# Performance work log

Measured on AMD Instinct MI355X. Metric: run time of the kernel, lower is better.

Reference implementation:

```python
import jax, jax.numpy as jnp
import numpy as np

T, B, H, I = 128, 32, 256, 256


def setup_inputs() -> dict:
    key = jax.random.key(0)
    ks = jax.random.split(key, 8)
    s = 0.05
    embs = jax.random.normal(ks[0], (T, B, I), jnp.float32)
    lens = jax.random.randint(ks[1], (B,), 1, T + 1)  # lengths in [1, T]
    W_ih = jax.random.normal(ks[2], (4 * H, I), jnp.float32) * s
    W_hh = jax.random.normal(ks[3], (4 * H, H), jnp.float32) * s
    b_ih = jax.random.normal(ks[4], (4 * H,), jnp.float32) * s
    b_hh = jax.random.normal(ks[5], (4 * H,), jnp.float32) * s
    W_a = jax.random.normal(ks[6], (H, 2 * H), jnp.float32) * s  # attention combine (Luong-style)
    b_a = jax.random.normal(ks[7], (H,), jnp.float32) * s
    return {"embs": embs, "lens": lens, "W_ih": W_ih, "W_hh": W_hh,
            "b_ih": b_ih, "b_hh": b_hh, "W_a": W_a, "b_a": b_a}


def reference(embs, lens, W_ih, W_hh, b_ih, b_hh, W_a, b_a):
    Tn, Bn, _ = embs.shape
    Hn = W_hh.shape[1]
    t_idx = jnp.arange(Tn)

    def step(carry, inp):
        h, c, buf, h_fin, c_fin = carry  # h,c: [B,H]; buf: [T,B,H] history of outputs
        t, emb = inp
        # dot-product attention of current hidden over past outputs (steps < t)
        scores = jnp.einsum('tbh,bh->tb', buf, h)
        valid = (t_idx < t)[:, None]
        alpha = jax.nn.softmax(jnp.where(valid, scores, -1e9), axis=0)
        ctx = jnp.einsum('tb,tbh->bh', alpha, buf)
        h_att = jnp.tanh(jnp.concatenate([ctx, h], axis=-1) @ W_a.T + b_a)
        h = jnp.where(t > 0, h_att, h)  # no history at t=0
        # standard PyTorch LSTM cell (gate order i,f,g,o)
        gates = emb @ W_ih.T + b_ih + h @ W_hh.T + b_hh
        i_g, f_g, g_g, o_g = jnp.split(gates, 4, axis=-1)
        c = jax.nn.sigmoid(f_g) * c + jax.nn.sigmoid(i_g) * jnp.tanh(g_g)
        h = jax.nn.sigmoid(o_g) * jnp.tanh(c)
        buf = buf.at[t].set(h)
        take = (t == lens - 1)[:, None]
        h_fin = jnp.where(take, h, h_fin)
        c_fin = jnp.where(take, c, c_fin)
        return (h, c, buf, h_fin, c_fin), h

    z = jnp.zeros((Bn, Hn), embs.dtype)
    buf0 = jnp.zeros((Tn, Bn, Hn), embs.dtype)
    carry, output = jax.lax.scan(step, (z, z, buf0, z, z), (t_idx, embs))
    # output: [T,B,H]; final (h,c) gathered at t == lens-1: [B,H]
    return output, carry[3], carry[4]
```

## Files before the change

kernel.cpp:

```cpp
#include <hip/hip_runtime.h>


#define T_DIM 128
#define B_DIM 32

typedef _Float16 half2_t __attribute__((ext_vector_type(2)));

static __device__ __forceinline__ unsigned pack2(float a, float b) {
  half2_t h;
  h.x = (_Float16)a;
  h.y = (_Float16)b;
  return __builtin_bit_cast(unsigned, h);
}

static __device__ __forceinline__ float dot2f(unsigned w, unsigned v, float acc) {
  half2_t a = __builtin_bit_cast(half2_t, w);
  half2_t b = __builtin_bit_cast(half2_t, v);
#if __has_builtin(__builtin_amdgcn_fdot2)
  return __builtin_amdgcn_fdot2(a, b, acc, false);
#else
  return acc + (float)a.x * (float)b.x + (float)a.y * (float)b.y;
#endif
}

static __device__ __forceinline__ float dot8(uint4 w, uint4 v, float acc) {
  acc = dot2f(w.x, v.x, acc);
  acc = dot2f(w.y, v.y, acc);
  acc = dot2f(w.z, v.z, acc);
  acc = dot2f(w.w, v.w, acc);
  return acc;
}

static __device__ __forceinline__ float lo16(unsigned u) {
  return (float)__builtin_bit_cast(half2_t, u).x;
}
static __device__ __forceinline__ float hi16(unsigned u) {
  return (float)__builtin_bit_cast(half2_t, u).y;
}

static __device__ __forceinline__ float fsig(float x) {
  return __builtin_amdgcn_rcpf(1.f + __expf(-x));
}
static __device__ __forceinline__ float ftanh(float x) {
  float e = __expf(2.f * x);
  return 1.f - 2.f * __builtin_amdgcn_rcpf(e + 1.f);
}

__global__ void pack_weights(const float* __restrict__ W_ih, const float* __restrict__ W_hh,
                             const float* __restrict__ W_a, float* __restrict__ W_ihT,
                             uint4* __restrict__ Whh_pack, uint4* __restrict__ Wa_pack,
                             unsigned long long* __restrict__ ywp,
                             unsigned long long* __restrict__ psx) {
  int n = blockIdx.x * 256 + threadIdx.x;
  {
    int k = n >> 10, r = n & 1023;
    W_ihT[n] = W_ih[r * 256 + k];
  }
  if (n < 32768) {
    int m = n >> 12, tid = (n >> 3) & 511, i = n & 7;
    int r_local = tid >> 2, qk = tid & 3;
    int q = r_local >> 5, jl = r_local & 31;
    int r = q * 256 + m * 32 + jl;
    const float* src = W_hh + r * 256 + (4 * i + qk) * 8;
    uint4 v;
    v.x = pack2(src[0], src[1]);
    v.y = pack2(src[2], src[3]);
    v.z = pack2(src[4], src[5]);
    v.w = pack2(src[6], src[7]);
    Whh_pack[n] = v;
  }
  if (n < 16384) {
    int m = n >> 11, j = (n >> 3) & 255, c = n & 7;
    int col0 = (c < 4) ? (m * 32 + c * 8) : (256 + m * 32 + (c - 4) * 8);
    const float* src = W_a + j * 512 + col0;
    uint4 v;
    v.x = pack2(src[0], src[1]);
    v.y = pack2(src[2], src[3]);
    v.z = pack2(src[4], src[5]);
    v.w = pack2(src[6], src[7]);
    Wa_pack[n] = v;
  }
  if (n < 65536)
    __hip_atomic_store(&ywp[n], 0ull, __ATOMIC_RELAXED, __HIP_MEMORY_SCOPE_AGENT);
  else if (n < 81920)
    __hip_atomic_store(&psx[n - 65536], 0ull, __ATOMIC_RELAXED, __HIP_MEMORY_SCOPE_AGENT);
}

__global__ void compute_gih(const float* __restrict__ embs, const float* __restrict__ W_ihT,
                            const float* __restrict__ b_ih, const float* __restrict__ b_hh,
                            float* __restrict__ gih) {
  __shared__ float embS[8][256];
  const int tid = threadIdx.x;
  const int tb0 = blockIdx.x * 8;
#pragma unroll
  for (int e = 0; e < 8; ++e) embS[e][tid] = embs[(size_t)(tb0 + e) * 256 + tid];
  __syncthreads();
  float acc[8][4];
#pragma unroll
  for (int e = 0; e < 8; ++e)
#pragma unroll
    for (int q = 0; q < 4; ++q) acc[e][q] = 0.f;
  for (int k = 0; k < 256; ++k) {
    float w0 = W_ihT[k * 1024 + tid];
    float w1 = W_ihT[k * 1024 + tid + 256];
    float w2 = W_ihT[k * 1024 + tid + 512];
    float w3 = W_ihT[k * 1024 + tid + 768];
#pragma unroll
    for (int e = 0; e < 8; ++e) {
      float x = embS[e][k];
      acc[e][0] += x * w0;
      acc[e][1] += x * w1;
      acc[e][2] += x * w2;
      acc[e][3] += x * w3;
    }
  }
#pragma unroll
  for (int q = 0; q < 4; ++q) {
    float bias = b_ih[q * 256 + tid] + b_hh[q * 256 + tid];
#pragma unroll
    for (int e = 0; e < 8; ++e)
      gih[(size_t)(tb0 + e) * 1024 + q * 256 + tid] = acc[e][q] + bias;
  }
}

__global__ void __launch_bounds__(512, 1)
alstm_rec(const int* __restrict__ lens, const float* __restrict__ gih,
          const uint4* __restrict__ Whh_pack, const uint4* __restrict__ Wa_pack,
          const float* __restrict__ b_a, unsigned long long* __restrict__ ywp,
          unsigned long long* __restrict__ psx, float* __restrict__ out,
          float* __restrict__ hfin, float* __restrict__ cfin) {
  const int tid = threadIdx.x;
  const int b = blockIdx.x & 31;
  const int m = blockIdx.x >> 5;

  __shared__ __align__(16) unsigned histSl[128 * 18];
  __shared__ __align__(16) float ystoreF[128 * 256];
  __shared__ __align__(16) unsigned hp2[128];
  __shared__ __align__(16) unsigned hsl2[16];
  __shared__ float sc[128];
  __shared__ float zp[4][256];
  __shared__ float gsl[128];

  uint4 wh4[8];
  {
    const uint4* p = Whh_pack + ((size_t)m * 512 + tid) * 8;
#pragma unroll
    for (int i = 0; i < 8; ++i) wh4[i] = p[i];
  }
  uint4 way[4], waw[4];
  {
    const int j_pub = (tid - 128) & 255;
    const uint4* p = Wa_pack + ((size_t)m * 256 + j_pub) * 8;
#pragma unroll
    for (int i = 0; i < 4; ++i) way[i] = p[i];
#pragma unroll
    for (int i = 0; i < 4; ++i) waw[i] = p[4 + i];
  }
  const float ba_j = (tid < 256) ? b_a[tid] : 0.f;
  const int len_b = lens[b];
  const int r_local = tid >> 2, qk = tid & 3;
  const int gq = r_local >> 5, gjl = r_local & 31;

  if (tid < 128) hp2[tid] = 0u;
  float c_reg = 0.f;
  __syncthreads();

  for (int t = 0; t < T_DIM; ++t) {
    float gih_v = gih[((size_t)t * 32 + b) * 1024 + gq * 256 + m * 32 + gjl];
    float w_j = 0.f;

    if (t > 0) {
      if (tid < 256) {
        const unsigned long long* base = ywp + b * 2048 + tid;
        unsigned long long v[8];
        for (;;) {
          bool ok = true;
#pragma unroll
          for (int mm = 0; mm < 8; ++mm)
            v[mm] = __hip_atomic_load(base + mm * 256, __ATOMIC_RELAXED, __HIP_MEMORY_SCOPE_AGENT);
#pragma unroll
          for (int mm = 0; mm < 8; ++mm) ok &= ((unsigned)v[mm] == (unsigned)t);
          if (ok) break;
          __builtin_amdgcn_s_sleep(1);
        }
        float y = 0.f, w = 0.f;
#pragma unroll
        for (int mm = 0; mm < 8; ++mm) {
          unsigned pl = (unsigned)(v[mm] >> 32);
          y += lo16(pl);
          w += hi16(pl);
        }
        w_j = w;
        ystoreF[(t - 1) * 256 + tid] = y;
      } else if (tid < 320) {
        const int p = tid - 256;
        const unsigned long long* base = psx + b * 512 + p;
        unsigned long long v[8];
        for (;;) {
          bool ok = true;
#pragma unroll
          for (int mm = 0; mm < 8; ++mm)
            v[mm] = __hip_atomic_load(base + mm * 64, __ATOMIC_RELAXED, __HIP_MEMORY_SCOPE_AGENT);
#pragma unroll
          for (int mm = 0; mm < 8; ++mm) ok &= ((unsigned)v[mm] == (unsigned)t);
          if (ok) break;
          __builtin_amdgcn_s_sleep(1);
        }
        float s0 = 0.f, s1 = 0.f;
#pragma unroll
        for (int mm = 0; mm < 8; ++mm) {
          unsigned pl = (unsigned)(v[mm] >> 32);
          s0 += lo16(pl);
          s1 += hi16(pl);
        }
        sc[2 * p] = s0;
        sc[2 * p + 1] = s1;
      }
      __syncthreads();
      if (tid < 64) {
        float v0 = (tid < t) ? sc[tid] : -3.0e38f;
        float v1 = (tid + 64 < t) ? sc[tid + 64] : -3.0e38f;
        float mx = fmaxf(v0, v1);
#pragma unroll
        for (int off = 32; off >= 1; off >>= 1) mx = fmaxf(mx, __shfl_xor(mx, off));
        float e0 = (tid < t) ? __expf(v0 - mx) : 0.f;
        float e1 = (tid + 64 < t) ? __expf(v1 - mx) : 0.f;
        float sm = e0 + e1;
#pragma unroll
        for (int off = 32; off >= 1; off >>= 1) sm += __shfl_xor(sm, off);
        float inv = __builtin_amdgcn_rcpf(sm);
        sc[tid] = e0 * inv;
        sc[tid + 64] = e1 * inv;
      }
      __syncthreads();
      {
        const int sp = tid >> 7, p2 = tid & 127;
        float c0 = 0.f, c1 = 0.f;
        const float* yb = ystoreF + 2 * p2;
        for (int s = sp; s < t; s += 4) {
          float al = sc[s];
          float2 yv = *(const float2*)(yb + s * 256);
          c0 += al * yv.x;
          c1 += al * yv.y;
        }
        zp[sp][2 * p2] = c0;
        zp[sp][2 * p2 + 1] = c1;
      }
      __syncthreads();
      if (tid < 256) {
        float z = zp[0][tid] + zp[1][tid] + zp[2][tid] + zp[3][tid];
        float hv = ftanh(ba_j + w_j + z);
        float o = __shfl_xor(hv, 1);
        if (!(tid & 1)) hp2[tid >> 1] = pack2(hv, o);
      }
      __syncthreads();
    }
    {
      float a = 0.f;
#pragma unroll
      for (int i = 0; i < 8; ++i) {
        const int c = 4 * i + qk;
        uint4 hv = *(const uint4*)&hp2[c << 2];
        a = dot8(wh4[i], hv, a);
      }
      a += __shfl_xor(a, 1);
      a += __shfl_xor(a, 2);
      if (qk == 0) gsl[r_local] = a + gih_v;
    }
    __syncthreads();
    if (tid < 32) {
      float ig = fsig(gsl[tid]);
      float fg = fsig(gsl[32 + tid]);
      float gg = ftanh(gsl[64 + tid]);
      float og = fsig(gsl[96 + tid]);
      float cn = fg * c_reg + ig * gg;
      float hn = og * ftanh(cn);
      c_reg = cn;
      out[((size_t)t * 32 + b) * 256 + m * 32 + tid] = hn;
      if (t == len_b - 1) {
        hfin[b * 256 + m * 32 + tid] = hn;
        cfin[b * 256 + m * 32 + tid] = cn;
      }
      float o = __shfl_xor(hn, 1);
      if (!(tid & 1)) {
        unsigned u = pack2(hn, o);
        hsl2[tid >> 1] = u;
        histSl[t * 18 + (tid >> 1)] = u;
      }
    }
    __syncthreads();
    if (tid < 128) {
      float a = 0.f;
#pragma unroll
      for (int k = 0; k < 8; ++k) {
        uint2 hw = *(const uint2*)&histSl[tid * 18 + 2 * k];
        uint2 qv = *(const uint2*)&hsl2[2 * k];
        a = dot2f(hw.x, qv.x, a);
        a = dot2f(hw.y, qv.y, a);
      }
      float o = __shfl_xor(a, 1);
      if (!(tid & 1)) {
        unsigned long long v = ((unsigned long long)pack2(a, o) << 32) |
                               (unsigned long long)(unsigned)(t + 1);
        __hip_atomic_store(&psx[b * 512 + m * 64 + (tid >> 1)], v, __ATOMIC_RELAXED,
                           __HIP_MEMORY_SCOPE_AGENT);
      }
    } else if (tid < 384) {
      const int j = tid - 128;
      float ay = 0.f, aw = 0.f;
#pragma unroll
      for (int c = 0; c < 4; ++c) {
        uint4 hv = *(const uint4*)&hsl2[c * 4];
        ay = dot8(way[c], hv, ay);
        aw = dot8(waw[c], hv, aw);
      }
      unsigned long long v = ((unsigned long long)pack2(ay, aw) << 32) |
                             (unsigned long long)(unsigned)(t + 1);
      __hip_atomic_store(&ywp[b * 2048 + m * 256 + j], v, __ATOMIC_RELAXED,
                         __HIP_MEMORY_SCOPE_AGENT);
    }
  }
}

extern "C" void kernel_launch(void* const* d_in, const int* in_sizes, int n_in,
                              void* d_out, int out_size, void* d_ws, size_t ws_size,
                              hipStream_t stream) {
  const float* embs = (const float*)d_in[0];
  const int* lens = (const int*)d_in[1];
  const float* W_ih = (const float*)d_in[2];
  const float* W_hh = (const float*)d_in[3];
  const float* b_ih = (const float*)d_in[4];
  const float* b_hh = (const float*)d_in[5];
  const float* W_a = (const float*)d_in[6];
  const float* b_a = (const float*)d_in[7];

  float* out = (float*)d_out;
  float* hfin = out + (size_t)T_DIM * B_DIM * 256;
  float* cfin = hfin + (size_t)B_DIM * 256;

  char* ws = (char*)d_ws;
  float* gih = (float*)ws;
  float* W_ihT = (float*)(ws + 16777216);
  uint4* Whh_pack = (uint4*)(ws + 17825792);
  uint4* Wa_pack = (uint4*)(ws + 18350080);
  unsigned long long* ywp = (unsigned long long*)(ws + 18612224);
  unsigned long long* psx = (unsigned long long*)(ws + 19136512);

  pack_weights<<<1024, 256, 0, stream>>>(W_ih, W_hh, W_a, W_ihT, Whh_pack, Wa_pack, ywp, psx);
  compute_gih<<<512, 256, 0, stream>>>(embs, W_ihT, b_ih, b_hh, gih);
  alstm_rec<<<256, 512, 0, stream>>>(lens, gih, Whh_pack, Wa_pack, b_a, ywp, psx, out, hfin,
                                     cfin);
}
```

Measured before the change: 564.0 us.

## Use fp16 dot2 for input projection and merge score/softmax passes

```diff
diff --git a/kernel.cpp b/kernel.cpp
--- a/kernel.cpp
+++ b/kernel.cpp
@@ -47,14 +47,15 @@
 }
 
 __global__ void pack_weights(const float* __restrict__ W_ih, const float* __restrict__ W_hh,
-                             const float* __restrict__ W_a, float* __restrict__ W_ihT,
+                             const float* __restrict__ W_a, unsigned* __restrict__ Wih16,
                              uint4* __restrict__ Whh_pack, uint4* __restrict__ Wa_pack,
                              unsigned long long* __restrict__ ywp,
                              unsigned long long* __restrict__ psx) {
   int n = blockIdx.x * 256 + threadIdx.x;
-  {
-    int k = n >> 10, r = n & 1023;
-    W_ihT[n] = W_ih[r * 256 + k];
+  if (n < 131072) {
+    int k2 = n >> 10, r = n & 1023;
+    const float* src = W_ih + r * 256 + 2 * k2;
+    Wih16[n] = pack2(src[0], src[1]);
   }
   if (n < 32768) {
     int m = n >> 12, tid = (n >> 3) & 511, i = n & 7;
@@ -86,39 +87,42 @@
     __hip_atomic_store(&psx[n - 65536], 0ull, __ATOMIC_RELAXED, __HIP_MEMORY_SCOPE_AGENT);
 }
 
-__global__ void compute_gih(const float* __restrict__ embs, const float* __restrict__ W_ihT,
+__global__ void compute_gih(const float* __restrict__ embs, const unsigned* __restrict__ Wih16,
                             const float* __restrict__ b_ih, const float* __restrict__ b_hh,
                             float* __restrict__ gih) {
-  __shared__ float embS[8][256];
+  __shared__ unsigned embS16[16][128];
   const int tid = threadIdx.x;
-  const int tb0 = blockIdx.x * 8;
-#pragma unroll
-  for (int e = 0; e < 8; ++e) embS[e][tid] = embs[(size_t)(tb0 + e) * 256 + tid];
+  const int tb0 = blockIdx.x * 16;
+  for (int x = tid; x < 2048; x += 256) {
+    int e = x >> 7, p = x & 127;
+    const float* s = embs + (size_t)(tb0 + e) * 256 + 2 * p;
+    embS16[e][p] = pack2(s[0], s[1]);
+  }
   __syncthreads();
-  float acc[8][4];
-#pragma unroll
-  for (int e = 0; e < 8; ++e)
+  float acc[16][4];
+#pragma unroll
+  for (int e = 0; e < 16; ++e)
 #pragma unroll
     for (int q = 0; q < 4; ++q) acc[e][q] = 0.f;
-  for (int k = 0; k < 256; ++k) {
-    float w0 = W_ihT[k * 1024 + tid];
-    float w1 = W_ihT[k * 1024 + tid + 256];
-    float w2 = W_ihT[k * 1024 + tid + 512];
-    float w3 = W_ihT[k * 1024 + tid + 768];
-#pragma unroll
-    for (int e = 0; e < 8; ++e) {
-      float x = embS[e][k];
-      acc[e][0] += x * w0;
-      acc[e][1] += x * w1;
-      acc[e][2] += x * w2;
-      acc[e][3] += x * w3;
+  for (int k2 = 0; k2 < 128; ++k2) {
+    unsigned w0 = Wih16[k2 * 1024 + tid];
+    unsigned w1 = Wih16[k2 * 1024 + tid + 256];
+    unsigned w2 = Wih16[k2 * 1024 + tid + 512];
+    unsigned w3 = Wih16[k2 * 1024 + tid + 768];
+#pragma unroll
+    for (int e = 0; e < 16; ++e) {
+      unsigned x = embS16[e][k2];
+      acc[e][0] = dot2f(w0, x, acc[e][0]);
+      acc[e][1] = dot2f(w1, x, acc[e][1]);
+      acc[e][2] = dot2f(w2, x, acc[e][2]);
+      acc[e][3] = dot2f(w3, x, acc[e][3]);
     }
   }
 #pragma unroll
   for (int q = 0; q < 4; ++q) {
     float bias = b_ih[q * 256 + tid] + b_hh[q * 256 + tid];
 #pragma unroll
-    for (int e = 0; e < 8; ++e)
+    for (int e = 0; e < 16; ++e)
       gih[(size_t)(tb0 + e) * 1024 + q * 256 + tid] = acc[e][q] + bias;
   }
 }
@@ -133,7 +137,7 @@
   const int b = blockIdx.x & 31;
   const int m = blockIdx.x >> 5;
 
-  __shared__ __align__(16) unsigned histSl[128 * 18];
+  __shared__ __align__(16) unsigned histSl[128 * 20];
   __shared__ __align__(16) float ystoreF[128 * 256];
   __shared__ __align__(16) unsigned hp2[128];
   __shared__ __align__(16) unsigned hsl2[16];
@@ -192,9 +196,9 @@
         }
         w_j = w;
         ystoreF[(t - 1) * 256 + tid] = y;
-      } else if (tid < 320) {
-        const int p = tid - 256;
-        const unsigned long long* base = psx + b * 512 + p;
+      } else if (tid >= 448) {
+        const int lane = tid - 448;
+        const unsigned long long* base = psx + b * 512 + lane;
         unsigned long long v[8];
         for (;;) {
           bool ok = true;
@@ -213,24 +217,19 @@
           s0 += lo16(pl);
           s1 += hi16(pl);
         }
-        sc[2 * p] = s0;
-        sc[2 * p + 1] = s1;
-      }
-      __syncthreads();
-      if (tid < 64) {
-        float v0 = (tid < t) ? sc[tid] : -3.0e38f;
-        float v1 = (tid + 64 < t) ? sc[tid + 64] : -3.0e38f;
+        float v0 = (2 * lane < t) ? s0 : -3.0e38f;
+        float v1 = (2 * lane + 1 < t) ? s1 : -3.0e38f;
         float mx = fmaxf(v0, v1);
 #pragma unroll
         for (int off = 32; off >= 1; off >>= 1) mx = fmaxf(mx, __shfl_xor(mx, off));
-        float e0 = (tid < t) ? __expf(v0 - mx) : 0.f;
-        float e1 = (tid + 64 < t) ? __expf(v1 - mx) : 0.f;
+        float e0 = (2 * lane < t) ? __expf(v0 - mx) : 0.f;
+        float e1 = (2 * lane + 1 < t) ? __expf(v1 - mx) : 0.f;
         float sm = e0 + e1;
 #pragma unroll
         for (int off = 32; off >= 1; off >>= 1) sm += __shfl_xor(sm, off);
         float inv = __builtin_amdgcn_rcpf(sm);
-        sc[tid] = e0 * inv;
-        sc[tid + 64] = e1 * inv;
+        sc[2 * lane] = e0 * inv;
+        sc[2 * lane + 1] = e1 * inv;
       }
       __syncthreads();
       {
@@ -268,44 +267,59 @@
       if (qk == 0) gsl[r_local] = a + gih_v;
     }
     __syncthreads();
-    if (tid < 32) {
-      float ig = fsig(gsl[tid]);
-      float fg = fsig(gsl[32 + tid]);
-      float gg = ftanh(gsl[64 + tid]);
-      float og = fsig(gsl[96 + tid]);
-      float cn = fg * c_reg + ig * gg;
-      float hn = og * ftanh(cn);
-      c_reg = cn;
-      out[((size_t)t * 32 + b) * 256 + m * 32 + tid] = hn;
-      if (t == len_b - 1) {
-        hfin[b * 256 + m * 32 + tid] = hn;
-        cfin[b * 256 + m * 32 + tid] = cn;
-      }
-      float o = __shfl_xor(hn, 1);
-      if (!(tid & 1)) {
-        unsigned u = pack2(hn, o);
-        hsl2[tid >> 1] = u;
-        histSl[t * 18 + (tid >> 1)] = u;
-      }
+    if (tid < 64) {
+      if (tid < 32) {
+        float ig = fsig(gsl[tid]);
+        float fg = fsig(gsl[32 + tid]);
+        float gg = ftanh(gsl[64 + tid]);
+        float og = fsig(gsl[96 + tid]);
+        float cn = fg * c_reg + ig * gg;
+        float hn = og * ftanh(cn);
+        c_reg = cn;
+        out[((size_t)t * 32 + b) * 256 + m * 32 + tid] = hn;
+        if (t == len_b - 1) {
+          hfin[b * 256 + m * 32 + tid] = hn;
+          cfin[b * 256 + m * 32 + tid] = cn;
+        }
+        float o = __shfl_xor(hn, 1);
+        if (!(tid & 1)) {
+          unsigned u = pack2(hn, o);
+          hsl2[tid >> 1] = u;
+          histSl[t * 20 + (tid >> 1)] = u;
+        }
+      }
+      uint4 q0 = *(const uint4*)&hsl2[0];
+      uint4 q1 = *(const uint4*)&hsl2[4];
+      uint4 q2 = *(const uint4*)&hsl2[8];
+      uint4 q3 = *(const uint4*)&hsl2[12];
+      const int r0 = 2 * tid, r1 = 2 * tid + 1;
+      float a0 = 0.f, a1 = 0.f;
+      {
+        uint4 h0, h1;
+        h0 = *(const uint4*)&histSl[r0 * 20 + 0];
+        h1 = *(const uint4*)&histSl[r1 * 20 + 0];
+        a0 = dot8(h0, q0, a0);
+        a1 = dot8(h1, q0, a1);
+        h0 = *(const uint4*)&histSl[r0 * 20 + 4];
+        h1 = *(const uint4*)&histSl[r1 * 20 + 4];
+        a0 = dot8(h0, q1, a0);
+        a1 = dot8(h1, q1, a1);
+        h0 = *(const uint4*)&histSl[r0 * 20 + 8];
+        h1 = *(const uint4*)&histSl[r1 * 20 + 8];
+        a0 = dot8(h0, q2, a0);
+        a1 = dot8(h1, q2, a1);
+        h0 = *(const uint4*)&histSl[r0 * 20 + 12];
+        h1 = *(const uint4*)&histSl[r1 * 20 + 12];
+        a0 = dot8(h0, q3, a0);
+        a1 = dot8(h1, q3, a1);
+      }
+      unsigned long long v = ((unsigned long long)pack2(a0, a1) << 32) |
+                             (unsigned long long)(unsigned)(t + 1);
+      __hip_atomic_store(&psx[b * 512 + m * 64 + tid], v, __ATOMIC_RELAXED,
+                         __HIP_MEMORY_SCOPE_AGENT);
     }
     __syncthreads();
-    if (tid < 128) {
-      float a = 0.f;
-#pragma unroll
-      for (int k = 0; k < 8; ++k) {
-        uint2 hw = *(const uint2*)&histSl[tid * 18 + 2 * k];
-        uint2 qv = *(const uint2*)&hsl2[2 * k];
-        a = dot2f(hw.x, qv.x, a);
-        a = dot2f(hw.y, qv.y, a);
-      }
-      float o = __shfl_xor(a, 1);
-      if (!(tid & 1)) {
-        unsigned long long v = ((unsigned long long)pack2(a, o) << 32) |
-                               (unsigned long long)(unsigned)(t + 1);
-        __hip_atomic_store(&psx[b * 512 + m * 64 + (tid >> 1)], v, __ATOMIC_RELAXED,
-                           __HIP_MEMORY_SCOPE_AGENT);
-      }
-    } else if (tid < 384) {
+    if (tid >= 128 && tid < 384) {
       const int j = tid - 128;
       float ay = 0.f, aw = 0.f;
 #pragma unroll
@@ -340,14 +354,14 @@
 
   char* ws = (char*)d_ws;
   float* gih = (float*)ws;
-  float* W_ihT = (float*)(ws + 16777216);
-  uint4* Whh_pack = (uint4*)(ws + 17825792);
-  uint4* Wa_pack = (uint4*)(ws + 18350080);
-  unsigned long long* ywp = (unsigned long long*)(ws + 18612224);
-  unsigned long long* psx = (unsigned long long*)(ws + 19136512);
-
-  pack_weights<<<1024, 256, 0, stream>>>(W_ih, W_hh, W_a, W_ihT, Whh_pack, Wa_pack, ywp, psx);
-  compute_gih<<<512, 256, 0, stream>>>(embs, W_ihT, b_ih, b_hh, gih);
+  unsigned* Wih16 = (unsigned*)(ws + 16777216);
+  uint4* Whh_pack = (uint4*)(ws + 17301504);
+  uint4* Wa_pack = (uint4*)(ws + 17825792);
+  unsigned long long* ywp = (unsigned long long*)(ws + 18087936);
+  unsigned long long* psx = (unsigned long long*)(ws + 18612224);
+
+  pack_weights<<<1024, 256, 0, stream>>>(W_ih, W_hh, W_a, Wih16, Whh_pack, Wa_pack, ywp, psx);
+  compute_gih<<<256, 256, 0, stream>>>(embs, Wih16, b_ih, b_hh, gih);
   alstm_rec<<<256, 512, 0, stream>>>(lens, gih, Whh_pack, Wa_pack, b_a, ywp, psx, out, hfin,
                                      cfin);
 }
```

Result: no change. 564.8 us (+0.1%).
